# Kernel optimization log

Measured on AMD Instinct MI355X. Metric: run time of the kernel, lower is better.

The kernel has to match this reference:

```python
import jax, jax.numpy as jnp
import numpy as np

N = 100000
E = 1600000
IN = 128
H = 256
K = 7          # n_hops + 1
INTERVAL = 3
R = K - INTERVAL + 1  # n_relations + 1 = 5


def setup_inputs() -> dict:
    key = jax.random.key(0)
    ks = jax.random.split(key, 8)
    features = jax.random.normal(ks[0], (N, IN), dtype=jnp.float32)
    W1 = jax.random.normal(ks[1], (K, IN, H), dtype=jnp.float32) * (1.0 / np.sqrt(IN))
    b1 = jnp.zeros((K, H), dtype=jnp.float32)
    W2 = jax.random.normal(ks[2], (K, H, H), dtype=jnp.float32) * (1.0 / np.sqrt(H))
    b2 = jnp.zeros((K, H), dtype=jnp.float32)
    Wr = jax.random.normal(ks[3], (R, H * INTERVAL, H), dtype=jnp.float32) * (1.0 / np.sqrt(H * INTERVAL))
    br = jnp.zeros((R, H), dtype=jnp.float32)
    row = jax.random.randint(ks[4], (E,), 0, N, dtype=jnp.int64)
    col = jax.random.randint(ks[5], (E,), 0, N, dtype=jnp.int64)
    return {"features": features, "W1": W1, "b1": b1, "W2": W2, "b2": b2,
            "Wr": Wr, "br": br, "row": row, "col": col}


def _norm_adj(row, col):
    # set_diag=True: add self loops; symm_norm: D^-1/2 (A+I) D^-1/2
    diag = jnp.arange(N, dtype=row.dtype)
    r = jnp.concatenate([row, diag])
    c = jnp.concatenate([col, diag])
    deg = jax.ops.segment_sum(jnp.ones_like(r, dtype=jnp.float32), r, num_segments=N)
    dinv = jnp.where(deg > 0, jax.lax.rsqrt(deg), 0.0)
    w = dinv[r] * dinv[c]  # [E+N]
    return r, c, w


def _forward(features, W1, b1, W2, b2, Wr, br, row, col):
    r, c, w = _norm_adj(row, col)

    def spmm(x):  # x: [N, F] -> A_hat @ x
        return jax.ops.segment_sum(x[c] * w[:, None], r, num_segments=N)

    def step(x, _):
        nx = spmm(x)
        return nx, nx

    _, hops = jax.lax.scan(step, features, None, length=K - 1)  # [K-1, N, IN]
    hop_feats = jnp.concatenate([features[None], hops], axis=0)  # [K, N, IN]

    # per-hop DeepSets (2-layer MLP with ReLU): [K, N, H]
    h = jax.nn.relu(jnp.einsum('kni,kih->knh', hop_feats, W1) + b1[:, None, :])
    h = jnp.einsum('knh,khg->kng', h, W2) + b2[:, None, :]

    hops_feats = jnp.transpose(h, (1, 0, 2))  # [N, K, H]
    # sliding windows of INTERVAL hops: [R, N, INTERVAL*H]
    wins = jnp.stack([hops_feats[:, i:i + INTERVAL, :].reshape(N, INTERVAL * H)
                      for i in range(R)], axis=0)
    rel = jax.nn.relu(jnp.einsum('rnd,rdh->rnh', wins, Wr) + br[:, None, :])  # [R, N, H]
    out = jnp.transpose(rel, (1, 0, 2)).reshape(N, R * H)  # concat over relations
    return out


def reference(features, W1, b1, W2, b2, Wr, br, row, col):
    return _forward(features, W1, b1, W2, b2, Wr, br, row, col)
```

## Files before the change

kernel.cpp:

```cpp
#include <hip/hip_runtime.h>

#define N_NODES 100000
#define E_EDGES 1600000
#define IN_F 128
#define H_F 256
#define K_HOPS 7
#define R_REL 5
#define OUT_W (R_REL * H_F)
#define SCAN_B ((N_NODES + 1023) / 1024)

typedef __attribute__((ext_vector_type(8))) short short8;
typedef __attribute__((ext_vector_type(4))) float f32x4;

#define GLOAD16(g, l) __builtin_amdgcn_global_load_lds( \
    (const __attribute__((address_space(1))) void*)(g), \
    (__attribute__((address_space(3))) void*)(l), 16, 0, 0)


__global__ void zero_int(int* __restrict__ p, int n) {
    int t = blockIdx.x * blockDim.x + threadIdx.x;
    if (t < n) p[t] = 0;
}

__global__ void deg_count(const int* __restrict__ row, int* __restrict__ deg) {
    int e = blockIdx.x * blockDim.x + threadIdx.x;
    if (e < E_EDGES) atomicAdd(&deg[row[e]], 1);
}

__global__ void dinv_compute(const int* __restrict__ deg, float* __restrict__ dinv) {
    int i = blockIdx.x * blockDim.x + threadIdx.x;
    if (i < N_NODES) dinv[i] = rsqrtf((float)(deg[i] + 1));
}

__global__ __launch_bounds__(1024) void scan1(const int* __restrict__ deg,
                                              int* __restrict__ rp, int* __restrict__ bsum) {
    __shared__ int ws[16];
    const int t = threadIdx.x, lane = t & 63, wv = t >> 6;
    int i = blockIdx.x * 1024 + t;
    int v = (i < N_NODES) ? deg[i] : 0;
    int x = v;
#pragma unroll
    for (int off = 1; off < 64; off <<= 1) {
        int n = __shfl_up(x, off, 64);
        if (lane >= off) x += n;
    }
    if (lane == 63) ws[wv] = x;
    __syncthreads();
    if (wv == 0 && lane < 16) {
        int s = ws[lane];
#pragma unroll
        for (int off = 1; off < 16; off <<= 1) {
            int n = __shfl_up(s, off, 64);
            if (lane >= off) s += n;
        }
        ws[lane] = s;
    }
    __syncthreads();
    int wbase = (wv == 0) ? 0 : ws[wv - 1];
    if (i < N_NODES) rp[i] = wbase + x - v;
    if (t == 1023) bsum[blockIdx.x] = ws[15];
}

__global__ __launch_bounds__(128) void scan2(int* __restrict__ bsum) {
    __shared__ int wtot[2];
    const int t = threadIdx.x, lane = t & 63, wv = t >> 6;
    int v = (t < SCAN_B) ? bsum[t] : 0;
    int x = v;
#pragma unroll
    for (int off = 1; off < 64; off <<= 1) {
        int n = __shfl_up(x, off, 64);
        if (lane >= off) x += n;
    }
    if (lane == 63) wtot[wv] = x;
    __syncthreads();
    int base = (wv == 1) ? wtot[0] : 0;
    if (t < SCAN_B) bsum[t] = base + x - v;
    if (t == 127) bsum[SCAN_B] = wtot[0] + wtot[1];
}

__global__ __launch_bounds__(1024) void scan3(int* __restrict__ rp,
                                              const int* __restrict__ bsum) {
    int i = blockIdx.x * 1024 + threadIdx.x;
    if (i < N_NODES) rp[i] += bsum[blockIdx.x];
    if (i == 0) rp[N_NODES] = bsum[SCAN_B];
}

__global__ void csr_scatter(const int* __restrict__ row, const int* __restrict__ col,
                            const float* __restrict__ dinv, const int* __restrict__ rowptr,
                            int* __restrict__ cursor, int* __restrict__ cols2,
                            float* __restrict__ ew) {
    int e = blockIdx.x * blockDim.x + threadIdx.x;
    if (e >= E_EDGES) return;
    int r = row[e], c = col[e];
    int pos = rowptr[r] + atomicAdd(&cursor[r], 1);
    cols2[pos] = c;
    ew[pos] = dinv[r] * dinv[c];
}

__global__ __launch_bounds__(256) void spmm_csr(
    const float4* __restrict__ x, const int* __restrict__ rowptr,
    const int* __restrict__ cols, const float* __restrict__ w,
    const float* __restrict__ dinv, float4* __restrict__ y) {
    const int wave = threadIdx.x >> 6, lane = threadIdx.x & 63;
    const int i = blockIdx.x * 4 + wave;
    if (i >= N_NODES) return;
    const int fh = lane & 31;
    const int slot = lane >> 5;
    const int jb = rowptr[i];
    const int cnt = rowptr[i + 1] - jb;

    float4 acc = make_float4(0.f, 0.f, 0.f, 0.f);
    int t = slot;
    for (; t + 6 < cnt; t += 8) {
        int c0 = cols[jb + t],     c1 = cols[jb + t + 2];
        int c2 = cols[jb + t + 4], c3 = cols[jb + t + 6];
        float ww0 = w[jb + t],     ww1 = w[jb + t + 2];
        float ww2 = w[jb + t + 4], ww3 = w[jb + t + 6];
        float4 v0 = x[(size_t)c0 * 32 + fh];
        float4 v1 = x[(size_t)c1 * 32 + fh];
        float4 v2 = x[(size_t)c2 * 32 + fh];
        float4 v3 = x[(size_t)c3 * 32 + fh];
        acc.x += ww0 * v0.x + ww1 * v1.x + ww2 * v2.x + ww3 * v3.x;
        acc.y += ww0 * v0.y + ww1 * v1.y + ww2 * v2.y + ww3 * v3.y;
        acc.z += ww0 * v0.z + ww1 * v1.z + ww2 * v2.z + ww3 * v3.z;
        acc.w += ww0 * v0.w + ww1 * v1.w + ww2 * v2.w + ww3 * v3.w;
    }
    for (; t < cnt; t += 2) {
        int c0 = cols[jb + t];
        float ww0 = w[jb + t];
        float4 v0 = x[(size_t)c0 * 32 + fh];
        acc.x += ww0 * v0.x;
        acc.y += ww0 * v0.y;
        acc.z += ww0 * v0.z;
        acc.w += ww0 * v0.w;
    }
    acc.x += __shfl_xor(acc.x, 32);
    acc.y += __shfl_xor(acc.y, 32);
    acc.z += __shfl_xor(acc.z, 32);
    acc.w += __shfl_xor(acc.w, 32);
    if (slot == 0) {
        float d = dinv[i];
        float s = d * d;
        float4 xv = x[(size_t)i * 32 + fh];
        acc.x += s * xv.x;
        acc.y += s * xv.y;
        acc.z += s * xv.z;
        acc.w += s * xv.w;
        y[(size_t)i * 32 + fh] = acc;
    }
}


__device__ __forceinline__ void f2bf_split(float v, short& h, short& l) {
    unsigned u = __float_as_uint(v);
    unsigned hb = (u + 0x7FFFu + ((u >> 16) & 1u)) >> 16;
    float fh = __uint_as_float(hb << 16);
    float r = v - fh;
    unsigned u2 = __float_as_uint(r);
    unsigned lb = (u2 + 0x7FFFu + ((u2 >> 16) & 1u)) >> 16;
    h = (short)(unsigned short)hb;
    l = (short)(unsigned short)lb;
}

__global__ __launch_bounds__(256) void wc_compute(const float* __restrict__ W2,
                                                  const float* __restrict__ Wr,
                                                  float* __restrict__ Wc) {
    __shared__ float as[8][256];
    const int z = blockIdx.x, j0 = blockIdx.y * 8, g = threadIdx.x;
    const int r = z / 3, d = z % 3, hop = r + d;
    const float* a = W2 + (size_t)hop * H_F * H_F + (size_t)j0 * H_F;
    for (int t = threadIdx.x; t < 8 * 256; t += 256)
        as[t >> 8][t & 255] = a[t];
    __syncthreads();
    const float* b = Wr + ((size_t)r * 768 + (size_t)d * H_F) * H_F + g;
    float acc[8] = {0.f, 0.f, 0.f, 0.f, 0.f, 0.f, 0.f, 0.f};
    for (int h = 0; h < H_F; ++h) {
        float bv = b[(size_t)h * H_F];
#pragma unroll
        for (int jj = 0; jj < 8; ++jj) acc[jj] += as[jj][h] * bv;
    }
#pragma unroll
    for (int jj = 0; jj < 8; ++jj)
        Wc[(size_t)z * H_F * H_F + (size_t)(j0 + jj) * H_F + g] = acc[jj];
}

__global__ __launch_bounds__(256) void bc_compute(const float* __restrict__ b2,
                                                  const float* __restrict__ Wr,
                                                  const float* __restrict__ br,
                                                  float* __restrict__ bc) {
    const int r = blockIdx.x, g = threadIdx.x;
    float acc = br[(size_t)r * H_F + g];
    for (int t = 0; t < 3 * H_F; ++t) {
        float bv = b2[(size_t)(r + t / H_F) * H_F + (t % H_F)];
        acc += bv * Wr[((size_t)r * 768 + t) * H_F + g];
    }
    bc[(size_t)r * H_F + g] = acc;
}

__global__ void transpose_convert(const float* __restrict__ in, short* __restrict__ oh,
                                  short* __restrict__ ol, int Kd, int grp) {
    __shared__ float t[32][33];
    const int i0 = blockIdx.x * 32, n0 = blockIdx.y * 32, z = blockIdx.z;
    const int tx = threadIdx.x, ty = threadIdx.y;
    const int outLd = grp * Kd;
    const float* ip = in + (size_t)z * Kd * 256;
#pragma unroll
    for (int j = 0; j < 4; ++j)
        t[ty + 8 * j][tx] = ip[(size_t)(i0 + ty + 8 * j) * 256 + n0 + tx];
    __syncthreads();
    size_t base = (size_t)(z / grp) * 256 * outLd + (size_t)(z % grp) * Kd;
#pragma unroll
    for (int j = 0; j < 4; ++j) {
        float v = t[tx][ty + 8 * j];
        short hb, lb;
        f2bf_split(v, hb, lb);
        size_t o = base + (size_t)(n0 + ty + 8 * j) * outLd + i0 + tx;
        oh[o] = hb;
        ol[o] = lb;
    }
}


#define LROW 40

__global__ __launch_bounds__(256, 2) void gemm_mlp(
    const float* __restrict__ A,
    const short* __restrict__ BTh, const short* __restrict__ BTl,
    short* __restrict__ Ch, short* __restrict__ Cl,
    const float* __restrict__ bias, int M)
{
    __shared__ short lds_buf[4 * 128 * LROW];
    short* Ah = lds_buf;
    short* Al = lds_buf + 128 * LROW;
    short* Bh = lds_buf + 2 * 128 * LROW;
    short* Bl = lds_buf + 3 * 128 * LROW;

    const int tid = threadIdx.x;
    const int lane = tid & 63, wave = tid >> 6;
    const int wm = wave & 1, wn = wave >> 1;
    const int fr = lane & 15, fg = lane >> 4;
    const int m0 = blockIdx.y * 128;
    const int n0 = blockIdx.x * 128;

    const int sr = tid >> 1;
    const int sc = (tid & 1) * 16;
    const bool avalid = (m0 + sr) < M;
    const int arow = avalid ? (m0 + sr) : (M - 1);

    f32x4 ga[4];
    short8 gbh[2], gbl[2];
    {
        const float* ap = A + (size_t)arow * IN_F + sc;
        const short* bph = BTh + (size_t)(n0 + sr) * IN_F + sc;
        const short* bpl = BTl + (size_t)(n0 + sr) * IN_F + sc;
#pragma unroll
        for (int l = 0; l < 4; ++l) ga[l] = *(const f32x4*)(ap + 4 * l);
        gbh[0] = *(const short8*)bph;  gbh[1] = *(const short8*)(bph + 8);
        gbl[0] = *(const short8*)bpl;  gbl[1] = *(const short8*)(bpl + 8);
    }

    f32x4 acc[4][4];
#pragma unroll
    for (int i = 0; i < 4; ++i)
#pragma unroll
        for (int j = 0; j < 4; ++j) acc[i][j] = (f32x4)0.f;

    const int nk = IN_F / 32;
    for (int kk = 0; kk < nk; ++kk) {
        __syncthreads();
        {
            short8 vh[2], vl[2];
#pragma unroll
            for (int l = 0; l < 4; ++l) {
                f32x4 v = ga[l];
                if (!avalid) v = (f32x4)0.f;
#pragma unroll
                for (int e = 0; e < 4; ++e) {
                    short hb, lb;
                    f2bf_split(v[e], hb, lb);
                    vh[l >> 1][(l & 1) * 4 + e] = hb;
                    vl[l >> 1][(l & 1) * 4 + e] = lb;
                }
            }
            *(short8*)(Ah + sr * LROW + sc)     = vh[0];
            *(short8*)(Ah + sr * LROW + sc + 8) = vh[1];
            *(short8*)(Al + sr * LROW + sc)     = vl[0];
            *(short8*)(Al + sr * LROW + sc + 8) = vl[1];
            *(short8*)(Bh + sr * LROW + sc)     = gbh[0];
            *(short8*)(Bh + sr * LROW + sc + 8) = gbh[1];
            *(short8*)(Bl + sr * LROW + sc)     = gbl[0];
            *(short8*)(Bl + sr * LROW + sc + 8) = gbl[1];
        }
        __syncthreads();

        if (kk + 1 < nk) {
            int k0 = (kk + 1) * 32;
            const float* ap = A + (size_t)arow * IN_F + k0 + sc;
            const short* bph = BTh + (size_t)(n0 + sr) * IN_F + k0 + sc;
            const short* bpl = BTl + (size_t)(n0 + sr) * IN_F + k0 + sc;
#pragma unroll
            for (int l = 0; l < 4; ++l) ga[l] = *(const f32x4*)(ap + 4 * l);
            gbh[0] = *(const short8*)(bph);  gbh[1] = *(const short8*)(bph + 8);
            gbl[0] = *(const short8*)(bpl);  gbl[1] = *(const short8*)(bpl + 8);
        }

        short8 afh[4], afl[4], bfh[4], bfl[4];
#pragma unroll
        for (int mf = 0; mf < 4; ++mf) {
            int r = wm * 64 + mf * 16 + fr;
            afh[mf] = *(const short8*)(Ah + r * LROW + fg * 8);
            afl[mf] = *(const short8*)(Al + r * LROW + fg * 8);
        }
#pragma unroll
        for (int nf = 0; nf < 4; ++nf) {
            int r = wn * 64 + nf * 16 + fr;
            bfh[nf] = *(const short8*)(Bh + r * LROW + fg * 8);
            bfl[nf] = *(const short8*)(Bl + r * LROW + fg * 8);
        }
#pragma unroll
        for (int mf = 0; mf < 4; ++mf)
#pragma unroll
            for (int nf = 0; nf < 4; ++nf) {
                acc[mf][nf] = __builtin_amdgcn_mfma_f32_16x16x32_bf16(
                    afh[mf], bfh[nf], acc[mf][nf], 0, 0, 0);
                acc[mf][nf] = __builtin_amdgcn_mfma_f32_16x16x32_bf16(
                    afh[mf], bfl[nf], acc[mf][nf], 0, 0, 0);
                acc[mf][nf] = __builtin_amdgcn_mfma_f32_16x16x32_bf16(
                    afl[mf], bfh[nf], acc[mf][nf], 0, 0, 0);
            }
    }

#pragma unroll
    for (int nf = 0; nf < 4; ++nf) {
        int colg = n0 + wn * 64 + nf * 16 + fr;
        float bv = bias[colg];
#pragma unroll
        for (int mf = 0; mf < 4; ++mf) {
            int rowbase = m0 + wm * 64 + mf * 16 + fg * 4;
#pragma unroll
            for (int j = 0; j < 4; ++j) {
                int rowg = rowbase + j;
                if (rowg < M) {
                    float v = fmaxf(acc[mf][nf][j] + bv, 0.f);
                    short hb, lb;
                    f2bf_split(v, hb, lb);
                    size_t idx = (size_t)rowg * H_F + colg;
                    Ch[idx] = hb;
                    Cl[idx] = lb;
                }
            }
        }
    }
}


__device__ __forceinline__ f32x4 mfma16(short8 a, short8 b, f32x4 c) {
    return __builtin_amdgcn_mfma_f32_16x16x32_bf16(a, b, c, 0, 0, 0);
}

template <int MFA, int MFB>
__device__ __forceinline__ void rel_phase(
    const short* Ahc, const short* Alc,
    const short8* bfh, const short8* bfl,
    f32x4 (&acc)[8][4], int wm, int fr, int fg)
{
    const int ra0 = wm * 128 + MFA * 16 + fr;
    const int ua0 = (fg + (ra0 >> 1)) & 3;
    short8 ahA = *(const short8*)(Ahc + ra0 * 32 + ua0 * 8);
    short8 alA = *(const short8*)(Alc + ra0 * 32 + ua0 * 8);
    const int ra1 = wm * 128 + MFB * 16 + fr;
    const int ua1 = (fg + (ra1 >> 1)) & 3;
    short8 ahB = *(const short8*)(Ahc + ra1 * 32 + ua1 * 8);
    short8 alB = *(const short8*)(Alc + ra1 * 32 + ua1 * 8);
    __builtin_amdgcn_sched_barrier(0);
    __builtin_amdgcn_s_barrier();
    asm volatile("s_waitcnt lgkmcnt(0)" ::: "memory");
    __builtin_amdgcn_sched_barrier(0);
    __builtin_amdgcn_s_setprio(1);
#pragma unroll
    for (int nf = 0; nf < 4; ++nf) {
        acc[MFA][nf] = mfma16(ahA, bfh[nf], acc[MFA][nf]);
        acc[MFA][nf] = mfma16(ahA, bfl[nf], acc[MFA][nf]);
        acc[MFA][nf] = mfma16(alA, bfh[nf], acc[MFA][nf]);
        acc[MFB][nf] = mfma16(ahB, bfh[nf], acc[MFB][nf]);
        acc[MFB][nf] = mfma16(ahB, bfl[nf], acc[MFB][nf]);
        acc[MFB][nf] = mfma16(alB, bfh[nf], acc[MFB][nf]);
    }
    __builtin_amdgcn_s_setprio(0);
    __builtin_amdgcn_sched_barrier(0);
    __builtin_amdgcn_s_barrier();
    __builtin_amdgcn_sched_barrier(0);
}

__global__ __launch_bounds__(512, 2) void gemm_rel(
    const short* __restrict__ h1h, const short* __restrict__ h1l, long hopStride,
    const short* __restrict__ wch, const short* __restrict__ wcl,
    float* __restrict__ outB, const float* __restrict__ bcB, int M, int nwg)
{
    __shared__ short lds[2][4][8192];

    const int bid = blockIdx.x;
    const int q8 = nwg >> 3, r8 = nwg & 7;
    const int xcd = bid & 7, idx = bid >> 3;
    const int wgid = (xcd < r8) ? (xcd * (q8 + 1) + idx)
                                : (r8 * (q8 + 1) + (xcd - r8) * q8 + idx);
    const int rrel = wgid % R_REL;
    const int mblk = wgid / R_REL;
    const int m0 = mblk * 256;

    const int tid = threadIdx.x;
    const int lane = tid & 63, wave = tid >> 6;
    const int wm = wave & 1, wn = wave >> 1;
    const int fr = lane & 15, fg = lane >> 4;

    const short* Agh = h1h + (size_t)rrel * hopStride;
    const short* Agl = h1l + (size_t)rrel * hopStride;
    const short* BTh = wch + (size_t)rrel * 256 * 768;
    const short* BTl = wcl + (size_t)rrel * 256 * 768;
    float* C = outB + (size_t)rrel * H_F;
    const float* bias = bcB + (size_t)rrel * H_F;

    const int kstart = ((3 - (rrel % 3)) % 3) * 8;

    int aoff[2], boff[2], loff[2];
#pragma unroll
    for (int p = 0; p < 2; ++p) {
        int c = wave * 2 + p;
        int r = c * 16 + (lane >> 2);
        int u = lane & 3;
        int g = (u - (r >> 1)) & 3;
        int ar = m0 + r; if (ar >= M) ar = M - 1;
        aoff[p] = ar * H_F + g * 8;
        boff[p] = r * 768 + g * 8;
        loff[p] = c * 512;
    }

#define STAGE_B4(buf, kg) do {                                                  \
        const short* bh_ = BTh + (kg);                                          \
        const short* bl_ = BTl + (kg);                                          \
        GLOAD16(bh_ + boff[0], &lds[buf][2][loff[0]]);                          \
        GLOAD16(bh_ + boff[1], &lds[buf][2][loff[1]]);                          \
        GLOAD16(bl_ + boff[0], &lds[buf][3][loff[0]]);                          \
        GLOAD16(bl_ + boff[1], &lds[buf][3][loff[1]]);                          \
    } while (0)

#define STAGE_A(buf, kg, p) do {                                                \
        int hop_ = (kg) >> 8, kin_ = (kg) & 255;                                \
        const short* ah_ = Agh + (size_t)hop_ * hopStride + kin_;               \
        const short* al_ = Agl + (size_t)hop_ * hopStride + kin_;               \
        GLOAD16(ah_ + aoff[p], &lds[buf][0][loff[p]]);                          \
        GLOAD16(al_ + aoff[p], &lds[buf][1][loff[p]]);                          \
    } while (0)

#define STAGE_FULL(buf, kg) do {                                                \
        STAGE_A(buf, kg, 0);                                                    \
        STAGE_A(buf, kg, 1);                                                    \
        STAGE_B4(buf, kg);                                                      \
    } while (0)

#define KIDX(t) ((((t) + kstart) % nk) * 32)

    f32x4 acc[8][4];
#pragma unroll
    for (int i = 0; i < 8; ++i)
#pragma unroll
        for (int j = 0; j < 4; ++j) acc[i][j] = (f32x4)0.f;

    const int nk = 768 / 32;
    const bool wodd = (wave & 1) != 0;

    STAGE_FULL(0, KIDX(0));
    STAGE_FULL(1, KIDX(1));

    int cur = 0;
    for (int kt = 0; kt < nk; ++kt) {
        const bool pf = (kt + 2 < nk);
        const int kg2 = KIDX(kt + 2);

        if (kt + 1 < nk) {
            asm volatile("s_waitcnt vmcnt(8)" ::: "memory");
        } else {
            asm volatile("s_waitcnt vmcnt(0)" ::: "memory");
        }
        __builtin_amdgcn_sched_barrier(0);
        __builtin_amdgcn_s_barrier();
        __builtin_amdgcn_sched_barrier(0);

        const short* Ahc = &lds[cur][0][0];
        const short* Alc = &lds[cur][1][0];
        const short* Bhc = &lds[cur][2][0];
        const short* Blc = &lds[cur][3][0];

        short8 bfh[4], bfl[4];
#pragma unroll
        for (int nf = 0; nf < 4; ++nf) {
            int rb = wn * 64 + nf * 16 + fr;
            int ub = (fg + (rb >> 1)) & 3;
            bfh[nf] = *(const short8*)(Bhc + rb * 32 + ub * 8);
            bfl[nf] = *(const short8*)(Blc + rb * 32 + ub * 8);
        }
        rel_phase<0, 4>(Ahc, Alc, bfh, bfl, acc, wm, fr, fg);

        if (pf) {
            STAGE_B4(cur, kg2);
            if (!wodd) STAGE_A(cur, kg2, 0);
        }
        rel_phase<1, 5>(Ahc, Alc, bfh, bfl, acc, wm, fr, fg);

        if (pf && !wodd) STAGE_A(cur, kg2, 1);
        rel_phase<2, 6>(Ahc, Alc, bfh, bfl, acc, wm, fr, fg);

        if (pf && wodd) STAGE_A(cur, kg2, 0);
        rel_phase<3, 7>(Ahc, Alc, bfh, bfl, acc, wm, fr, fg);

        if (pf && wodd) STAGE_A(cur, kg2, 1);

        cur ^= 1;
    }

#pragma unroll
    for (int nf = 0; nf < 4; ++nf) {
        int colg = wn * 64 + nf * 16 + fr;
        float bv = bias[colg];
#pragma unroll
        for (int mf = 0; mf < 8; ++mf) {
            int rowbase = m0 + wm * 128 + mf * 16 + fg * 4;
#pragma unroll
            for (int j = 0; j < 4; ++j) {
                int rowg = rowbase + j;
                if (rowg < M)
                    C[(size_t)rowg * OUT_W + colg] = fmaxf(acc[mf][nf][j] + bv, 0.f);
            }
        }
    }
#undef STAGE_B4
#undef STAGE_A
#undef STAGE_FULL
#undef KIDX
}


template <int MODE>
__global__ __launch_bounds__(256, 2) void gemm_presplit(
    const short* __restrict__ Agh, const short* __restrict__ Agl, int lda,
    const short* __restrict__ BTh, const short* __restrict__ BTl, int ldb, int Kd,
    float* __restrict__ C, int ldc, const float* __restrict__ bias, int M)
{
    __shared__ short lds_buf[4 * 128 * LROW];
    short* Ah = lds_buf;
    short* Al = lds_buf + 128 * LROW;
    short* Bh = lds_buf + 2 * 128 * LROW;
    short* Bl = lds_buf + 3 * 128 * LROW;

    const int tid = threadIdx.x;
    const int lane = tid & 63, wave = tid >> 6;
    const int wm = wave & 1, wn = wave >> 1;
    const int fr = lane & 15, fg = lane >> 4;
    const int m0 = blockIdx.y * 128;
    const int n0 = blockIdx.x * 128;

    const int sr = tid >> 1;
    const int sc = (tid & 1) * 16;
    const bool avalid = (m0 + sr) < M;
    const int arow = avalid ? (m0 + sr) : (M - 1);

    short8 gah[2], gal[2], gbh[2], gbl[2];
    {
        const short* aph = Agh + (size_t)arow * lda + sc;
        const short* apl = Agl + (size_t)arow * lda + sc;
        const short* bph = BTh + (size_t)(n0 + sr) * ldb + sc;
        const short* bpl = BTl + (size_t)(n0 + sr) * ldb + sc;
        gah[0] = *(const short8*)aph;  gah[1] = *(const short8*)(aph + 8);
        gal[0] = *(const short8*)apl;  gal[1] = *(const short8*)(apl + 8);
        gbh[0] = *(const short8*)bph;  gbh[1] = *(const short8*)(bph + 8);
        gbl[0] = *(const short8*)bpl;  gbl[1] = *(const short8*)(bpl + 8);
    }

    f32x4 acc[4][4];
#pragma unroll
    for (int i = 0; i < 4; ++i)
#pragma unroll
        for (int j = 0; j < 4; ++j) acc[i][j] = (f32x4)0.f;

    const int nk = Kd / 32;
    for (int kk = 0; kk < nk; ++kk) {
        __syncthreads();
        *(short8*)(Ah + sr * LROW + sc)     = gah[0];
        *(short8*)(Ah + sr * LROW + sc + 8) = gah[1];
        *(short8*)(Al + sr * LROW + sc)     = gal[0];
        *(short8*)(Al + sr * LROW + sc + 8) = gal[1];
        *(short8*)(Bh + sr * LROW + sc)     = gbh[0];
        *(short8*)(Bh + sr * LROW + sc + 8) = gbh[1];
        *(short8*)(Bl + sr * LROW + sc)     = gbl[0];
        *(short8*)(Bl + sr * LROW + sc + 8) = gbl[1];
        __syncthreads();

        if (kk + 1 < nk) {
            int k0 = (kk + 1) * 32;
            const short* aph = Agh + (size_t)arow * lda + k0 + sc;
            const short* apl = Agl + (size_t)arow * lda + k0 + sc;
            const short* bph = BTh + (size_t)(n0 + sr) * ldb + k0 + sc;
            const short* bpl = BTl + (size_t)(n0 + sr) * ldb + k0 + sc;
            gah[0] = *(const short8*)aph;  gah[1] = *(const short8*)(aph + 8);
            gal[0] = *(const short8*)apl;  gal[1] = *(const short8*)(apl + 8);
            gbh[0] = *(const short8*)bph;  gbh[1] = *(const short8*)(bph + 8);
            gbl[0] = *(const short8*)bpl;  gbl[1] = *(const short8*)(bpl + 8);
        }

        short8 afh[4], afl[4], bfh[4], bfl[4];
#pragma unroll
        for (int mf = 0; mf < 4; ++mf) {
            int r = wm * 64 + mf * 16 + fr;
            afh[mf] = *(const short8*)(Ah + r * LROW + fg * 8);
            afl[mf] = *(const short8*)(Al + r * LROW + fg * 8);
        }
#pragma unroll
        for (int nf = 0; nf < 4; ++nf) {
            int r = wn * 64 + nf * 16 + fr;
            bfh[nf] = *(const short8*)(Bh + r * LROW + fg * 8);
            bfl[nf] = *(const short8*)(Bl + r * LROW + fg * 8);
        }
#pragma unroll
        for (int mf = 0; mf < 4; ++mf)
#pragma unroll
            for (int nf = 0; nf < 4; ++nf) {
                acc[mf][nf] = __builtin_amdgcn_mfma_f32_16x16x32_bf16(
                    afh[mf], bfh[nf], acc[mf][nf], 0, 0, 0);
                acc[mf][nf] = __builtin_amdgcn_mfma_f32_16x16x32_bf16(
                    afh[mf], bfl[nf], acc[mf][nf], 0, 0, 0);
                acc[mf][nf] = __builtin_amdgcn_mfma_f32_16x16x32_bf16(
                    afl[mf], bfh[nf], acc[mf][nf], 0, 0, 0);
            }
    }

#pragma unroll
    for (int nf = 0; nf < 4; ++nf) {
        int colg = n0 + wn * 64 + nf * 16 + fr;
        float bv = (MODE == 0) ? bias[colg] : 0.f;
#pragma unroll
        for (int mf = 0; mf < 4; ++mf) {
            int rowbase = m0 + wm * 64 + mf * 16 + fg * 4;
#pragma unroll
            for (int j = 0; j < 4; ++j) {
                int rowg = rowbase + j;
                if (rowg < M) {
                    size_t idx = (size_t)rowg * ldc + colg;
                    float v = acc[mf][nf][j] + bv;
                    if (MODE >= 2) v += C[idx];
                    if (MODE & 1) v = fmaxf(v, 0.f);
                    C[idx] = v;
                }
            }
        }
    }
}


extern "C" void kernel_launch(void* const* d_in, const int* in_sizes, int n_in,
                              void* d_out, int out_size, void* d_ws, size_t ws_size,
                              hipStream_t stream) {
    const float* features = (const float*)d_in[0];
    const float* W1 = (const float*)d_in[1];
    const float* b1 = (const float*)d_in[2];
    const float* W2 = (const float*)d_in[3];
    const float* b2 = (const float*)d_in[4];
    const float* Wr = (const float*)d_in[5];
    const float* br = (const float*)d_in[6];
    const int* row = (const int*)d_in[7];
    const int* col = (const int*)d_in[8];
    float* out = (float*)d_out;

    char* ws = (char*)d_ws;
    int* deg = (int*)ws;
    int* rowptr = (int*)(ws + (1ull << 20));
    float* dinv = (float*)(ws + (2ull << 20));
    int* bsum = (int*)(ws + (3ull << 20));
    int* cols2 = (int*)(ws + (4ull << 20));
    float* ew = (float*)(ws + (11ull << 20));
    short* w1h = (short*)(ws + (18ull << 20));
    short* w1l = (short*)(ws + (19ull << 20));
    float* wc32 = (float*)(ws + (20ull << 20));
    short* wch = (short*)(ws + (24ull << 20));
    short* wcl = (short*)(ws + (26ull << 20));
    float* bc = (float*)(ws + (28ull << 20));
    float* xa = (float*)(ws + (32ull << 20));
    float* xb = (float*)(ws + (96ull << 20));
    short* h1h = (short*)(ws + (160ull << 20));
    short* h1l = (short*)(ws + (576ull << 20));

    const bool windowed = ws_size >= (1000ull << 20);

    zero_int<<<(N_NODES + 255) / 256, 256, 0, stream>>>(deg, N_NODES);
    deg_count<<<(E_EDGES + 255) / 256, 256, 0, stream>>>(row, deg);
    dinv_compute<<<(N_NODES + 255) / 256, 256, 0, stream>>>(deg, dinv);
    scan1<<<SCAN_B, 1024, 0, stream>>>(deg, rowptr, bsum);
    scan2<<<1, 128, 0, stream>>>(bsum);
    scan3<<<SCAN_B, 1024, 0, stream>>>(rowptr, bsum);
    zero_int<<<(N_NODES + 255) / 256, 256, 0, stream>>>(deg, N_NODES);
    csr_scatter<<<(E_EDGES + 255) / 256, 256, 0, stream>>>(row, col, dinv, rowptr,
                                                           deg, cols2, ew);

    wc_compute<<<dim3(15, 32), 256, 0, stream>>>(W2, Wr, wc32);
    bc_compute<<<R_REL, 256, 0, stream>>>(b2, Wr, br, bc);

    dim3 tb(32, 8);
    transpose_convert<<<dim3(IN_F / 32, 8, K_HOPS), tb, 0, stream>>>(W1, w1h, w1l, IN_F, 1);
    transpose_convert<<<dim3(H_F / 32, 8, 15), tb, 0, stream>>>(wc32, wch, wcl, H_F, 3);

    const float* xcur = features;
    float* bufs[2] = {xa, xb};
    for (int k = 0; k < K_HOPS; ++k) {
        short* h1hd = windowed ? (h1h + (size_t)k * N_NODES * H_F) : h1h;
        short* h1ld = windowed ? (h1l + (size_t)k * N_NODES * H_F) : h1l;
        dim3 grid(2, (N_NODES + 127) / 128);
        gemm_mlp<<<grid, 256, 0, stream>>>(xcur, w1h + (size_t)k * 256 * IN_F,
                                           w1l + (size_t)k * 256 * IN_F,
                                           h1hd, h1ld, b1 + (size_t)k * H_F, N_NODES);

        if (!windowed) {
            int rlo = (k - 2 < 0) ? 0 : (k - 2);
            int rhi = (k < R_REL - 1) ? k : (R_REL - 1);
            for (int r = rlo; r <= rhi; ++r) {
                int d = k - r;
                const short* Bh = wch + (size_t)r * 256 * 768 + (size_t)d * H_F;
                const short* Bl = wcl + (size_t)r * 256 * 768 + (size_t)d * H_F;
                float* Cp = out + (size_t)r * H_F;
                if (k == r)
                    gemm_presplit<0><<<grid, 256, 0, stream>>>(
                        h1h, h1l, H_F, Bh, Bl, 768, H_F, Cp, OUT_W,
                        bc + (size_t)r * H_F, N_NODES);
                else if (k == r + 2)
                    gemm_presplit<3><<<grid, 256, 0, stream>>>(
                        h1h, h1l, H_F, Bh, Bl, 768, H_F, Cp, OUT_W, nullptr, N_NODES);
                else
                    gemm_presplit<2><<<grid, 256, 0, stream>>>(
                        h1h, h1l, H_F, Bh, Bl, 768, H_F, Cp, OUT_W, nullptr, N_NODES);
            }
        }

        if (k < K_HOPS - 1) {
            float* xn = bufs[k & 1];
            spmm_csr<<<(N_NODES + 3) / 4, 256, 0, stream>>>(
                (const float4*)xcur, rowptr, cols2, ew, dinv, (float4*)xn);
            xcur = xn;
        }
    }

    if (windowed) {
        int mblocks = (N_NODES + 255) / 256;
        int nwg = mblocks * R_REL;
        gemm_rel<<<nwg, 512, 0, stream>>>(h1h, h1l, (long)N_NODES * H_F,
                                          wch, wcl, out, bc, N_NODES, nwg);
    }
}
```

Measured before the change: 2.148 ms.

## Stage MLP layer-1 epilogue through LDS for coalesced stores; nontemporal CSR loads

```diff
diff --git a/kernel.cpp b/kernel.cpp
--- a/kernel.cpp
+++ b/kernel.cpp
@@ -112,10 +112,14 @@
     float4 acc = make_float4(0.f, 0.f, 0.f, 0.f);
     int t = slot;
     for (; t + 6 < cnt; t += 8) {
-        int c0 = cols[jb + t],     c1 = cols[jb + t + 2];
-        int c2 = cols[jb + t + 4], c3 = cols[jb + t + 6];
-        float ww0 = w[jb + t],     ww1 = w[jb + t + 2];
-        float ww2 = w[jb + t + 4], ww3 = w[jb + t + 6];
+        int c0 = __builtin_nontemporal_load(&cols[jb + t]);
+        int c1 = __builtin_nontemporal_load(&cols[jb + t + 2]);
+        int c2 = __builtin_nontemporal_load(&cols[jb + t + 4]);
+        int c3 = __builtin_nontemporal_load(&cols[jb + t + 6]);
+        float ww0 = __builtin_nontemporal_load(&w[jb + t]);
+        float ww1 = __builtin_nontemporal_load(&w[jb + t + 2]);
+        float ww2 = __builtin_nontemporal_load(&w[jb + t + 4]);
+        float ww3 = __builtin_nontemporal_load(&w[jb + t + 6]);
         float4 v0 = x[(size_t)c0 * 32 + fh];
         float4 v1 = x[(size_t)c1 * 32 + fh];
         float4 v2 = x[(size_t)c2 * 32 + fh];
@@ -330,25 +334,55 @@
             }
     }
 
+    short hfrag[4][4][4], lfrag[4][4][4];
 #pragma unroll
     for (int nf = 0; nf < 4; ++nf) {
         int colg = n0 + wn * 64 + nf * 16 + fr;
         float bv = bias[colg];
 #pragma unroll
-        for (int mf = 0; mf < 4; ++mf) {
-            int rowbase = m0 + wm * 64 + mf * 16 + fg * 4;
+        for (int mf = 0; mf < 4; ++mf)
 #pragma unroll
             for (int j = 0; j < 4; ++j) {
-                int rowg = rowbase + j;
+                float v = fmaxf(acc[mf][nf][j] + bv, 0.f);
+                f2bf_split(v, hfrag[mf][nf][j], lfrag[mf][nf][j]);
+            }
+    }
+    __syncthreads();
+
+    short* ldsS = lds_buf;
+    const int crow = tid >> 2;
+    const int cchk = (tid & 3) * 32;
+#pragma unroll
+    for (int half = 0; half < 2; ++half) {
+#pragma unroll
+        for (int hl = 0; hl < 2; ++hl) {
+            if (wm == half) {
+#pragma unroll
+                for (int nf = 0; nf < 4; ++nf) {
+                    int col = wn * 64 + nf * 16 + fr;
+#pragma unroll
+                    for (int mf = 0; mf < 4; ++mf) {
+                        int rl = mf * 16 + fg * 4;
+#pragma unroll
+                        for (int j = 0; j < 4; ++j)
+                            ldsS[(rl + j) * 128 + col] =
+                                hl ? lfrag[mf][nf][j] : hfrag[mf][nf][j];
+                    }
+                }
+            }
+            __syncthreads();
+            {
+                int rowg = m0 + half * 64 + crow;
                 if (rowg < M) {
-                    float v = fmaxf(acc[mf][nf][j] + bv, 0.f);
-                    short hb, lb;
-                    f2bf_split(v, hb, lb);
-                    size_t idx = (size_t)rowg * H_F + colg;
-                    Ch[idx] = hb;
-                    Cl[idx] = lb;
+                    short* dst = (hl ? Cl : Ch) + (size_t)rowg * H_F + n0 + cchk;
+                    const short* src = ldsS + crow * 128 + cchk;
+                    *(short8*)(dst)      = *(const short8*)(src);
+                    *(short8*)(dst + 8)  = *(const short8*)(src + 8);
+                    *(short8*)(dst + 16) = *(const short8*)(src + 16);
+                    *(short8*)(dst + 24) = *(const short8*)(src + 24);
                 }
             }
+            __syncthreads();
         }
     }
 }
```

Result: faster. 2.020 ms (-6.0%).
